# Optimization experiments

Hardware: AMD Instinct MI355X
Metric: run time of the kernel (lower is better)

## Reference

```python
import jax, jax.numpy as jnp
import numpy as np

N = 100000      # num_nodes
E = 600000      # edges per relation
R = 3           # num_relations
F_IN = 128
F_OUT = 64


def setup_inputs() -> dict:
    key = jax.random.key(0)
    k0, k1, k2, k3 = jax.random.split(key, 4)
    x = jax.random.normal(k0, (N, F_IN), dtype=jnp.float32)
    edge_indices = jax.random.randint(k1, (R, 2, E), 0, N, dtype=jnp.int32)
    # torch.randperm per relation -> fixed permutations as int inputs
    perms = jnp.stack([jax.random.permutation(jax.random.fold_in(k2, r), N).astype(jnp.int32)
                       for r in range(R)])
    # GCNConv glorot weight + zero bias, one per relation
    Ws = jax.random.normal(k3, (R, F_IN, F_OUT), dtype=jnp.float32) * (1.0 / np.sqrt(F_IN))
    bs = jnp.zeros((R, F_OUT), dtype=jnp.float32)
    return {"x": x, "edge_indices": edge_indices, "perms": perms, "Ws": Ws, "bs": bs}


def gcn_conv(h, src, dst, W, b, n):
    """PyG GCNConv: add self-loops, sym-normalize, linear, scatter-sum, bias."""
    loops = jnp.arange(n, dtype=src.dtype)
    s = jnp.concatenate([src, loops])
    d = jnp.concatenate([dst, loops])
    deg = jax.ops.segment_sum(jnp.ones_like(s, dtype=h.dtype), d, num_segments=n)
    dinv = jnp.where(deg > 0, jax.lax.rsqrt(deg), 0.0)
    norm = dinv[s] * dinv[d]                      # [E+n]
    hw = h @ W                                    # [n, F_OUT]
    out = jax.ops.segment_sum(hw[s] * norm[:, None], d, num_segments=n)
    return out + b


def reference(x, edge_indices, perms, Ws, bs):
    # Eval mode: F.dropout(p=0.5, training=False) is identity.
    n = x.shape[0]
    pos_hs, neg_hs, summaries = [], [], []
    for r in range(R):
        src, dst = edge_indices[r, 0], edge_indices[r, 1]
        pos_h = jax.nn.relu(gcn_conv(x, src, dst, Ws[r], bs[r], n))
        neg_h = jax.nn.relu(gcn_conv(x[perms[r]], src, dst, Ws[r], bs[r], n))
        pos_hs.append(pos_h)
        neg_hs.append(neg_h)
        summaries.append(pos_h.mean(axis=0, keepdims=True))
    return (jnp.stack(pos_hs), jnp.stack(neg_hs), jnp.stack(summaries))
```

## Files before the change

### kernel.cpp

```cpp
#include <hip/hip_runtime.h>

#define F_IN 128
#define F_OUT 64
#define NCHUNK 256

typedef float f32x2 __attribute__((ext_vector_type(2)));

__device__ __forceinline__ unsigned short f2bf(float f) {
    unsigned int u = __float_as_uint(f);
    u += 0x7fff + ((u >> 16) & 1);
    return (unsigned short)(u >> 16);
}
__device__ __forceinline__ float bf2f(unsigned short s) {
    return __uint_as_float((unsigned int)s << 16);
}

__global__ __launch_bounds__(256) void deg_kernel(const int* __restrict__ ei,
                                                  int* __restrict__ deg,
                                                  int N, int E) {
    int r = blockIdx.y;
    int e = blockIdx.x * 256 + threadIdx.x;
    if (e >= E) return;
    int d = ei[(size_t)r * 2 * E + E + e];
    atomicAdd(&deg[(size_t)r * N + d], 1);
}

__global__ __launch_bounds__(256) void invperm_kernel(const int* __restrict__ perm,
                                                      int* __restrict__ ip, int N) {
    int r = blockIdx.y;
    int i = blockIdx.x * 256 + threadIdx.x;
    if (i >= N) return;
    ip[(size_t)r * N + perm[(size_t)r * N + i]] = i;
}

__global__ __launch_bounds__(256) void scan_partial(const int* __restrict__ deg,
                                                    int* __restrict__ psum,
                                                    int N, int chunk) {
    int r = blockIdx.y, b = blockIdx.x;
    int start = b * chunk, end = min(start + chunk, N);
    int s = 0;
    for (int i = start + threadIdx.x; i < end; i += 256)
        s += deg[(size_t)r * N + i];
    __shared__ int ls[256];
    ls[threadIdx.x] = s;
    __syncthreads();
    for (int off = 128; off > 0; off >>= 1) {
        if (threadIdx.x < off) ls[threadIdx.x] += ls[threadIdx.x + off];
        __syncthreads();
    }
    if (threadIdx.x == 0) psum[r * NCHUNK + b] = ls[0];
}

__global__ __launch_bounds__(256) void scan_offsets(int* __restrict__ psum,
                                                    int* __restrict__ rowstart,
                                                    int N, int R) {
    int tid = threadIdx.x, lane = tid & 63, wv = tid >> 6;
    __shared__ int wsum[4];
    for (int r = 0; r < R; ++r) {
        int v = psum[r * NCHUNK + tid];
        int sc = v;
        #pragma unroll
        for (int off = 1; off < 64; off <<= 1) {
            int t = __shfl_up(sc, off, 64);
            if (lane >= off) sc += t;
        }
        if (lane == 63) wsum[wv] = sc;
        __syncthreads();
        int woff = 0;
        for (int w = 0; w < wv; ++w) woff += wsum[w];
        psum[r * NCHUNK + tid] = woff + sc - v;
        if (tid == 255) rowstart[(size_t)r * (N + 1) + N] = woff + sc;
        __syncthreads();
    }
}

__global__ __launch_bounds__(256) void scan_apply(int* __restrict__ deg,
                                                  const int* __restrict__ psum,
                                                  int* __restrict__ rowstart,
                                                  float* __restrict__ dinv,
                                                  int N, int chunk) {
    int r = blockIdx.y, b = blockIdx.x;
    int tid = threadIdx.x, lane = tid & 63, wv = tid >> 6;
    int start = b * chunk, end = min(start + chunk, N);
    int* dg = deg + (size_t)r * N;
    int* rs = rowstart + (size_t)r * (N + 1);
    float* dv = dinv + (size_t)r * N;
    __shared__ int wsum[4];
    int v[4]; int tsum = 0;
    #pragma unroll
    for (int j = 0; j < 4; ++j) {
        int idx = start + tid * 4 + j;
        v[j] = (idx < end) ? dg[idx] : 0;
        tsum += v[j];
    }
    int sc = tsum;
    #pragma unroll
    for (int off = 1; off < 64; off <<= 1) {
        int t = __shfl_up(sc, off, 64);
        if (lane >= off) sc += t;
    }
    if (lane == 63) wsum[wv] = sc;
    __syncthreads();
    int woff = 0;
    for (int w = 0; w < wv; ++w) woff += wsum[w];
    int excl = psum[r * NCHUNK + b] + woff + sc - tsum;
    #pragma unroll
    for (int j = 0; j < 4; ++j) {
        int idx = start + tid * 4 + j;
        if (idx < end) {
            rs[idx] = excl;
            dg[idx] = excl;
            dv[idx] = rsqrtf((float)(v[j] + 1));
        }
        excl += v[j];
    }
}

__global__ __launch_bounds__(256) void fill_csr(const int* __restrict__ ei,
                                                const float* __restrict__ dinv,
                                                int* __restrict__ cursor,
                                                int2* __restrict__ csr,
                                                int N, int E) {
    int r = blockIdx.y;
    int e = blockIdx.x * 256 + threadIdx.x;
    if (e >= E) return;
    const int* base = ei + (size_t)r * 2 * E;
    int s = base[e], d = base[E + e];
    const float* dv = dinv + (size_t)r * N;
    float nrm = dv[s] * dv[d];
    int pos = atomicAdd(&cursor[(size_t)r * N + d], 1);
    int2 sp; sp.x = s; sp.y = __float_as_int(nrm);
    csr[(size_t)r * E + pos] = sp;
}

__global__ __launch_bounds__(256) void gemm_xw(const float* __restrict__ x,
                                               const float* __restrict__ W,
                                               const int* __restrict__ ip,
                                               unsigned short* __restrict__ combined,
                                               int N) {
    __shared__ float xs[64 * 68];
    __shared__ float wsd[128 * 68];
    int r = blockIdx.y;
    const float* Wr = W + (size_t)r * F_IN * F_OUT;
    {
        int k = threadIdx.x >> 1, cq = threadIdx.x & 1;
        const float* wrow = Wr + k * F_OUT;
        #pragma unroll
        for (int j = 0; j < 8; ++j) {
            int col = (cq + 2 * j) * 4;
            *(float4*)&wsd[k * 68 + col] = *(const float4*)(wrow + col);
        }
    }
    int row0 = blockIdx.x * 64;
    int ty = threadIdx.x >> 4, tx = threadIdx.x & 15;
    int lrow = threadIdx.x >> 2;
    int kq = threadIdx.x & 3;
    int grow = row0 + lrow; if (grow >= N) grow = N - 1;
    const float* xrow = x + (size_t)grow * F_IN;
    float acc[4][4] = {};
    for (int kc = 0; kc < 2; ++kc) {
        __syncthreads();
        #pragma unroll
        for (int j = 0; j < 4; ++j) {
            int kk4 = kq + 4 * j;
            float4 v = *(const float4*)(xrow + kc * 64 + kk4 * 4);
            xs[(kk4 * 4 + 0) * 68 + lrow] = v.x;
            xs[(kk4 * 4 + 1) * 68 + lrow] = v.y;
            xs[(kk4 * 4 + 2) * 68 + lrow] = v.z;
            xs[(kk4 * 4 + 3) * 68 + lrow] = v.w;
        }
        __syncthreads();
        const float* wk = &wsd[kc * 64 * 68];
        #pragma unroll 8
        for (int kk = 0; kk < 64; ++kk) {
            float4 xa = *(const float4*)&xs[kk * 68 + ty * 4];
            float4 wb = *(const float4*)&wk[kk * 68 + tx * 4];
            acc[0][0] += xa.x * wb.x; acc[0][1] += xa.x * wb.y;
            acc[0][2] += xa.x * wb.z; acc[0][3] += xa.x * wb.w;
            acc[1][0] += xa.y * wb.x; acc[1][1] += xa.y * wb.y;
            acc[1][2] += xa.y * wb.z; acc[1][3] += xa.y * wb.w;
            acc[2][0] += xa.z * wb.x; acc[2][1] += xa.z * wb.y;
            acc[2][2] += xa.z * wb.z; acc[2][3] += xa.z * wb.w;
            acc[3][0] += xa.w * wb.x; acc[3][1] += xa.w * wb.y;
            acc[3][2] += xa.w * wb.z; acc[3][3] += xa.w * wb.w;
        }
    }
    const int* ipr = ip + (size_t)r * N;
    #pragma unroll
    for (int i = 0; i < 4; ++i) {
        int orow = row0 + ty * 4 + i;
        if (orow < N) {
            ushort4 v;
            v.x = f2bf(acc[i][0]); v.y = f2bf(acc[i][1]);
            v.z = f2bf(acc[i][2]); v.w = f2bf(acc[i][3]);
            size_t rb = (size_t)r * N;
            *(ushort4*)(combined + (rb + orow) * 128 + tx * 4) = v;
            int j = ipr[orow];
            *(ushort4*)(combined + (rb + j) * 128 + 64 + tx * 4) = v;
        }
    }
}

__global__ __launch_bounds__(256) void gather_kernel(const int2* __restrict__ csr,
                                                     const int* __restrict__ rowstart,
                                                     const float* __restrict__ dinv,
                                                     const unsigned short* __restrict__ combined,
                                                     const float* __restrict__ bs,
                                                     float* __restrict__ out_pos,
                                                     float* __restrict__ out_neg,
                                                     float* __restrict__ partial,
                                                     int N, int E) {
    int r = blockIdx.y;
    int lane = threadIdx.x & 63, wv = threadIdx.x >> 6;
    int i = blockIdx.x * 4 + wv;
    i = __builtin_amdgcn_readfirstlane(i);
    int c0 = (lane & 31) * 2;
    __shared__ float ls[4][64];
    float p0 = 0.f, p1 = 0.f;
    if (i < N) {
        const unsigned short* cw = combined + (size_t)r * N * 128;
        const int* rs = rowstart + (size_t)r * (N + 1);
        int j0 = rs[i], j1 = rs[i + 1];
        j0 = __builtin_amdgcn_readfirstlane(j0);
        j1 = __builtin_amdgcn_readfirstlane(j1);
        float di = dinv[(size_t)r * N + i];
        float w = di * di;
        unsigned int sv = *(const unsigned int*)(cw + (size_t)i * 128 + 2 * lane);
        float acc0 = bf2f((unsigned short)sv) * w;
        float acc1 = bf2f((unsigned short)(sv >> 16)) * w;
        const int2* cs = csr + (size_t)r * E;
        int last = j1 - 1;
        for (int j = j0; j < j1; j += 8) {
            int2 e[8];
            float nm[8];
            #pragma unroll
            for (int k = 0; k < 8; ++k) {
                int idx = j + k;
                int ic = idx < last ? idx : last;
                e[k] = cs[ic];
                nm[k] = (idx < j1) ? __int_as_float(e[k].y) : 0.f;
            }
            #pragma unroll
            for (int k = 0; k < 8; ++k) {
                unsigned int v = *(const unsigned int*)(cw + (size_t)e[k].x * 128 + 2 * lane);
                acc0 += bf2f((unsigned short)v) * nm[k];
                acc1 += bf2f((unsigned short)(v >> 16)) * nm[k];
            }
        }
        float2 bv = *(const float2*)(bs + r * F_OUT + c0);
        float q0 = acc0 + bv.x; q0 = q0 > 0.f ? q0 : 0.f;
        float q1 = acc1 + bv.y; q1 = q1 > 0.f ? q1 : 0.f;
        size_t off = (size_t)r * N * F_OUT + (size_t)i * F_OUT + c0;
        float* dst = (lane < 32) ? (out_pos + off) : (out_neg + off);
        f32x2 o; o.x = q0; o.y = q1;
        __builtin_nontemporal_store(o, (f32x2*)dst);
        if (lane < 32) { p0 = q0; p1 = q1; }
    }
    if (lane < 32) { ls[wv][c0] = p0; ls[wv][c0 + 1] = p1; }
    __syncthreads();
    if (wv == 0) {
        float t = ls[0][lane] + ls[1][lane] + ls[2][lane] + ls[3][lane];
        atomicAdd(&partial[((size_t)r * 256 + (blockIdx.x & 255)) * F_OUT + lane], t);
    }
}

__global__ __launch_bounds__(256) void summary_reduce(const float* __restrict__ partial,
                                                      float* __restrict__ summary,
                                                      float inv_n) {
    int r = blockIdx.x;
    int lane = threadIdx.x & 63, wv = threadIdx.x >> 6;
    __shared__ float ls[256];
    float s = 0.f;
    for (int c = wv; c < 256; c += 4)
        s += partial[((size_t)r * 256 + c) * F_OUT + lane];
    ls[threadIdx.x] = s;
    __syncthreads();
    if (wv == 0)
        summary[r * F_OUT + lane] =
            (ls[lane] + ls[64 + lane] + ls[128 + lane] + ls[192 + lane]) * inv_n;
}

extern "C" void kernel_launch(void* const* d_in, const int* in_sizes, int n_in,
                              void* d_out, int out_size, void* d_ws, size_t ws_size,
                              hipStream_t stream) {
    const float* x    = (const float*)d_in[0];
    const int*   ei   = (const int*)d_in[1];
    const int*   perm = (const int*)d_in[2];
    const float* Ws   = (const float*)d_in[3];
    const float* bs   = (const float*)d_in[4];

    const int N = in_sizes[0] / F_IN;
    const int R = in_sizes[4] / F_OUT;
    const int E = in_sizes[1] / (2 * R);

    float* out_pos = (float*)d_out;
    float* out_neg = out_pos + (size_t)R * N * F_OUT;
    float* summary = out_neg + (size_t)R * N * F_OUT;

    char* ws = (char*)d_ws;
    size_t off = 0;
    auto alloc = [&](size_t bytes) { void* p = ws + off;
        off += (bytes + 255) & ~(size_t)255; return p; };
    int*   deg      = (int*)  alloc((size_t)R * N * 4);
    float* dinv     = (float*)alloc((size_t)R * N * 4);
    int*   rowstart = (int*)  alloc((size_t)R * (N + 1) * 4);
    int*   ip       = (int*)  alloc((size_t)R * N * 4);
    int2*  csr      = (int2*) alloc((size_t)R * E * 8);
    unsigned short* combined = (unsigned short*)alloc((size_t)R * N * 128 * 2);
    float* partial  = (float*)alloc((size_t)R * 256 * F_OUT * 4);
    int*   psum     = (int*)  alloc((size_t)R * NCHUNK * 4);

    const int chunk = (N + NCHUNK - 1) / NCHUNK;

    hipMemsetAsync(deg, 0, (size_t)R * N * sizeof(int), stream);
    hipMemsetAsync(partial, 0, (size_t)R * 256 * F_OUT * sizeof(float), stream);

    deg_kernel<<<dim3((E + 255) / 256, R), 256, 0, stream>>>(ei, deg, N, E);
    invperm_kernel<<<dim3((N + 255) / 256, R), 256, 0, stream>>>(perm, ip, N);
    scan_partial<<<dim3(NCHUNK, R), 256, 0, stream>>>(deg, psum, N, chunk);
    scan_offsets<<<1, 256, 0, stream>>>(psum, rowstart, N, R);
    scan_apply<<<dim3(NCHUNK, R), 256, 0, stream>>>(deg, psum, rowstart, dinv, N, chunk);
    fill_csr<<<dim3((E + 255) / 256, R), 256, 0, stream>>>(ei, dinv, deg, csr, N, E);
    gemm_xw<<<dim3((N + 63) / 64, R), 256, 0, stream>>>(x, Ws, ip, combined, N);
    gather_kernel<<<dim3((N + 3) / 4, R), 256, 0, stream>>>(csr, rowstart, dinv,
                                                            combined, bs, out_pos,
                                                            out_neg, partial, N, E);
    summary_reduce<<<R, 256, 0, stream>>>(partial, summary, 1.0f / (float)N);
}
```

Baseline: 543.1 us.

## Replace FP32 SIMT GEMM with split-bf16 MFMA GEMM covering all relations

Replaces the scalar FP32 x·W kernel with an MFMA bf16 kernel that splits each FP32 operand into hi and lo bf16 parts and sums three products, keeping close to FP32 accuracy. Each block loads its 128 rows of x once into shared memory and loops over all three relations, so x is read from global memory once instead of once per relation. A small pre-kernel converts and transposes W into hi/lo bf16 form. The cost is three MFMAs per tile, larger shared memory (about 68 KB) that may lower occupancy, and W fragments read straight from global memory.

```diff
diff --git a/kernel.cpp b/kernel.cpp
--- a/kernel.cpp
+++ b/kernel.cpp
@@ -5,6 +5,8 @@
 #define NCHUNK 256
 
 typedef float f32x2 __attribute__((ext_vector_type(2)));
+typedef float f32x4 __attribute__((ext_vector_type(4)));
+typedef short bf16x8 __attribute__((ext_vector_type(8)));
 
 __device__ __forceinline__ unsigned short f2bf(float f) {
     unsigned int u = __float_as_uint(f);
@@ -133,70 +135,110 @@
     csr[(size_t)r * E + pos] = sp;
 }
 
-__global__ __launch_bounds__(256) void gemm_xw(const float* __restrict__ x,
-                                               const float* __restrict__ W,
-                                               const int* __restrict__ ip,
-                                               unsigned short* __restrict__ combined,
-                                               int N) {
-    __shared__ float xs[64 * 68];
-    __shared__ float wsd[128 * 68];
-    int r = blockIdx.y;
-    const float* Wr = W + (size_t)r * F_IN * F_OUT;
+__global__ __launch_bounds__(256) void w_convert(const float* __restrict__ W,
+                                                 unsigned short* __restrict__ wt_hi,
+                                                 unsigned short* __restrict__ wt_lo,
+                                                 int R) {
+    int idx = blockIdx.x * 256 + threadIdx.x;
+    if (idx >= R * 64 * 128) return;
+    int k = idx & 127, c = (idx >> 7) & 63, r = idx >> 13;
+    float v = W[((size_t)r * F_IN + k) * F_OUT + c];
+    unsigned short h = f2bf(v);
+    wt_hi[idx] = h;
+    wt_lo[idx] = f2bf(v - bf2f(h));
+}
+
+__global__ __launch_bounds__(256) void gemm_xw_mfma(const float* __restrict__ x,
+                                                    const unsigned short* __restrict__ wt_hi,
+                                                    const unsigned short* __restrict__ wt_lo,
+                                                    const int* __restrict__ ip,
+                                                    unsigned short* __restrict__ combined,
+                                                    int N, int R) {
+    constexpr int KP = 136;
+    __shared__ __align__(16) unsigned short xs_hi[128 * KP];
+    __shared__ __align__(16) unsigned short xs_lo[128 * KP];
+
+    int row0 = blockIdx.x * 128;
+    int tid = threadIdx.x;
     {
-        int k = threadIdx.x >> 1, cq = threadIdx.x & 1;
-        const float* wrow = Wr + k * F_OUT;
-        #pragma unroll
-        for (int j = 0; j < 8; ++j) {
-            int col = (cq + 2 * j) * 4;
-            *(float4*)&wsd[k * 68 + col] = *(const float4*)(wrow + col);
-        }
-    }
-    int row0 = blockIdx.x * 64;
-    int ty = threadIdx.x >> 4, tx = threadIdx.x & 15;
-    int lrow = threadIdx.x >> 2;
-    int kq = threadIdx.x & 3;
-    int grow = row0 + lrow; if (grow >= N) grow = N - 1;
-    const float* xrow = x + (size_t)grow * F_IN;
-    float acc[4][4] = {};
-    for (int kc = 0; kc < 2; ++kc) {
-        __syncthreads();
-        #pragma unroll
-        for (int j = 0; j < 4; ++j) {
-            int kk4 = kq + 4 * j;
-            float4 v = *(const float4*)(xrow + kc * 64 + kk4 * 4);
-            xs[(kk4 * 4 + 0) * 68 + lrow] = v.x;
-            xs[(kk4 * 4 + 1) * 68 + lrow] = v.y;
-            xs[(kk4 * 4 + 2) * 68 + lrow] = v.z;
-            xs[(kk4 * 4 + 3) * 68 + lrow] = v.w;
-        }
-        __syncthreads();
-        const float* wk = &wsd[kc * 64 * 68];
-        #pragma unroll 8
-        for (int kk = 0; kk < 64; ++kk) {
-            float4 xa = *(const float4*)&xs[kk * 68 + ty * 4];
-            float4 wb = *(const float4*)&wk[kk * 68 + tx * 4];
-            acc[0][0] += xa.x * wb.x; acc[0][1] += xa.x * wb.y;
-            acc[0][2] += xa.x * wb.z; acc[0][3] += xa.x * wb.w;
-            acc[1][0] += xa.y * wb.x; acc[1][1] += xa.y * wb.y;
-            acc[1][2] += xa.y * wb.z; acc[1][3] += xa.y * wb.w;
-            acc[2][0] += xa.z * wb.x; acc[2][1] += xa.z * wb.y;
-            acc[2][2] += xa.z * wb.z; acc[2][3] += xa.z * wb.w;
-            acc[3][0] += xa.w * wb.x; acc[3][1] += xa.w * wb.y;
-            acc[3][2] += xa.w * wb.z; acc[3][3] += xa.w * wb.w;
-        }
-    }
-    const int* ipr = ip + (size_t)r * N;
-    #pragma unroll
-    for (int i = 0; i < 4; ++i) {
-        int orow = row0 + ty * 4 + i;
-        if (orow < N) {
-            ushort4 v;
-            v.x = f2bf(acc[i][0]); v.y = f2bf(acc[i][1]);
-            v.z = f2bf(acc[i][2]); v.w = f2bf(acc[i][3]);
-            size_t rb = (size_t)r * N;
-            *(ushort4*)(combined + (rb + orow) * 128 + tx * 4) = v;
-            int j = ipr[orow];
-            *(ushort4*)(combined + (rb + j) * 128 + 64 + tx * 4) = v;
+        int rr = tid >> 1, half = tid & 1;
+        int grow = row0 + rr; if (grow >= N) grow = N - 1;
+        const float* xr = x + (size_t)grow * F_IN + half * 64;
+        unsigned short* dh = &xs_hi[rr * KP + half * 64];
+        unsigned short* dl = &xs_lo[rr * KP + half * 64];
+        #pragma unroll
+        for (int c = 0; c < 64; c += 4) {
+            float4 v = *(const float4*)(xr + c);
+            unsigned short h0 = f2bf(v.x), h1 = f2bf(v.y),
+                           h2 = f2bf(v.z), h3 = f2bf(v.w);
+            ushort4 hv; hv.x = h0; hv.y = h1; hv.z = h2; hv.w = h3;
+            *(ushort4*)(dh + c) = hv;
+            ushort4 lv;
+            lv.x = f2bf(v.x - bf2f(h0)); lv.y = f2bf(v.y - bf2f(h1));
+            lv.z = f2bf(v.z - bf2f(h2)); lv.w = f2bf(v.w - bf2f(h3));
+            *(ushort4*)(dl + c) = lv;
+        }
+    }
+    __syncthreads();
+
+    int wv = tid >> 6, lane = tid & 63;
+    int l15 = lane & 15, lhi = lane >> 4;
+    int nbase = wv * 32;
+    for (int r = 0; r < R; ++r) {
+        f32x4 acc[2][4];
+        #pragma unroll
+        for (int nt = 0; nt < 2; ++nt)
+            #pragma unroll
+            for (int ct = 0; ct < 4; ++ct)
+                acc[nt][ct] = (f32x4){0.f, 0.f, 0.f, 0.f};
+        const unsigned short* wh = wt_hi + (size_t)r * 64 * 128;
+        const unsigned short* wl = wt_lo + (size_t)r * 64 * 128;
+        #pragma unroll
+        for (int kc = 0; kc < 4; ++kc) {
+            int kb = kc * 32 + lhi * 8;
+            bf16x8 bh[2], bl[2], ah[4], al[4];
+            #pragma unroll
+            for (int nt = 0; nt < 2; ++nt) {
+                int ro = (nbase + nt * 16 + l15) * KP + kb;
+                bh[nt] = *(const bf16x8*)&xs_hi[ro];
+                bl[nt] = *(const bf16x8*)&xs_lo[ro];
+            }
+            #pragma unroll
+            for (int ct = 0; ct < 4; ++ct) {
+                int wo = (ct * 16 + l15) * 128 + kb;
+                ah[ct] = *(const bf16x8*)(wh + wo);
+                al[ct] = *(const bf16x8*)(wl + wo);
+            }
+            #pragma unroll
+            for (int ct = 0; ct < 4; ++ct)
+                #pragma unroll
+                for (int nt = 0; nt < 2; ++nt) {
+                    acc[nt][ct] = __builtin_amdgcn_mfma_f32_16x16x32_bf16(
+                        ah[ct], bh[nt], acc[nt][ct], 0, 0, 0);
+                    acc[nt][ct] = __builtin_amdgcn_mfma_f32_16x16x32_bf16(
+                        ah[ct], bl[nt], acc[nt][ct], 0, 0, 0);
+                    acc[nt][ct] = __builtin_amdgcn_mfma_f32_16x16x32_bf16(
+                        al[ct], bh[nt], acc[nt][ct], 0, 0, 0);
+                }
+        }
+        const int* ipr = ip + (size_t)r * N;
+        size_t rb = (size_t)r * N;
+        #pragma unroll
+        for (int nt = 0; nt < 2; ++nt) {
+            int xrow = row0 + nbase + nt * 16 + l15;
+            if (xrow < N) {
+                int nrow = ipr[xrow];
+                #pragma unroll
+                for (int ct = 0; ct < 4; ++ct) {
+                    f32x4 a = acc[nt][ct];
+                    ushort4 v;
+                    v.x = f2bf(a.x); v.y = f2bf(a.y);
+                    v.z = f2bf(a.z); v.w = f2bf(a.w);
+                    int cb = ct * 16 + lhi * 4;
+                    *(ushort4*)(combined + (rb + xrow) * 128 + cb) = v;
+                    *(ushort4*)(combined + (rb + nrow) * 128 + 64 + cb) = v;
+                }
+            }
         }
     }
 }
@@ -309,6 +351,8 @@
     unsigned short* combined = (unsigned short*)alloc((size_t)R * N * 128 * 2);
     float* partial  = (float*)alloc((size_t)R * 256 * F_OUT * 4);
     int*   psum     = (int*)  alloc((size_t)R * NCHUNK * 4);
+    unsigned short* wt_hi = (unsigned short*)alloc((size_t)R * 64 * 128 * 2);
+    unsigned short* wt_lo = (unsigned short*)alloc((size_t)R * 64 * 128 * 2);
 
     const int chunk = (N + NCHUNK - 1) / NCHUNK;
 
@@ -317,11 +361,12 @@
 
     deg_kernel<<<dim3((E + 255) / 256, R), 256, 0, stream>>>(ei, deg, N, E);
     invperm_kernel<<<dim3((N + 255) / 256, R), 256, 0, stream>>>(perm, ip, N);
+    w_convert<<<(R * 64 * 128 + 255) / 256, 256, 0, stream>>>(Ws, wt_hi, wt_lo, R);
     scan_partial<<<dim3(NCHUNK, R), 256, 0, stream>>>(deg, psum, N, chunk);
     scan_offsets<<<1, 256, 0, stream>>>(psum, rowstart, N, R);
     scan_apply<<<dim3(NCHUNK, R), 256, 0, stream>>>(deg, psum, rowstart, dinv, N, chunk);
     fill_csr<<<dim3((E + 255) / 256, R), 256, 0, stream>>>(ei, dinv, deg, csr, N, E);
-    gemm_xw<<<dim3((N + 63) / 64, R), 256, 0, stream>>>(x, Ws, ip, combined, N);
+    gemm_xw_mfma<<<(N + 127) / 128, 256, 0, stream>>>(x, wt_hi, wt_lo, ip, combined, N, R);
     gather_kernel<<<dim3((N + 3) / 4, R), 256, 0, stream>>>(csr, rowstart, dinv,
                                                             combined, bs, out_pos,
                                                             out_neg, partial, N, E);
```

After: 548.5 us. Within noise of the previous version (+1.0%).
